# Kernel tuning notes

Hardware: AMD Instinct MI355X
Metric: run time of the kernel (lower is better)

Reference implementation:

```python
import jax, jax.numpy as jnp
import numpy as np

B, S, QD, KD = 8, 8192, 1024, 1024
AD = min(QD, KD)
EPS = 1e-5


def _ste(x, xq):
    # straight-through estimator: forward uses xq, gradient flows as identity
    return x + jax.lax.stop_gradient(xq - x)


def bitlinear(x, w, b):
    """BitNet b1.58-style BitLinear: ternary per-tensor weight quant,
    per-token int8 absmax activation quant, both with STE."""
    s = jnp.mean(jnp.abs(w)) + EPS                      # per-tensor weight scale
    wq = _ste(w, jnp.clip(jnp.round(w / s), -1.0, 1.0) * s)
    g = jnp.max(jnp.abs(x), axis=-1, keepdims=True) + EPS  # per-token act scale
    xq = _ste(x, jnp.clip(jnp.round(x * (127.0 / g)), -128.0, 127.0) * (g / 127.0))
    return jnp.matmul(xq, wq.T) + b


def setup_inputs() -> dict:
    key = jax.random.key(0)
    ks = jax.random.split(key, 6)
    sc = 0.02
    return {
        "query": jax.random.normal(ks[0], (B, QD), dtype=jnp.float32),
        "context_memory": jax.random.normal(ks[1], (B, S, KD), dtype=jnp.float32),
        "w_q": jax.random.normal(ks[2], (AD, QD), dtype=jnp.float32) * sc,
        "b_q": jnp.zeros((AD,), dtype=jnp.float32),
        "w_k": jax.random.normal(ks[3], (AD, KD), dtype=jnp.float32) * sc,
        "b_k": jnp.zeros((AD,), dtype=jnp.float32),
        "w_v": jax.random.normal(ks[4], (QD, KD), dtype=jnp.float32) * sc,
        "b_v": jnp.zeros((QD,), dtype=jnp.float32),
        "w_c": jax.random.normal(ks[5], (QD, 2 * QD), dtype=jnp.float32) * sc,
        "b_c": jnp.zeros((QD,), dtype=jnp.float32),
    }


def reference(query, context_memory, w_q, b_q, w_k, b_k, w_v, b_v, w_c, b_c):
    attention_dim = w_q.shape[0]
    q = bitlinear(query, w_q, b_q)                 # [B, A]
    k = bitlinear(context_memory, w_k, b_k)        # [B, S, A]
    v = bitlinear(context_memory, w_v, b_v)        # [B, S, QD]
    scores = jnp.einsum('ba,bsa->bs', q, k) / (attention_dim ** 0.5)
    attn = jax.nn.softmax(scores, axis=-1)         # [B, S]
    ctx = jnp.einsum('bs,bsq->bq', attn, v)        # [B, QD]
    combined = jnp.concatenate([query, ctx], axis=-1)  # [B, 2*QD]
    return bitlinear(combined, w_c, b_c)           # [B, QD]
```

## Files before the change

### kernel.cpp

```cpp
#include <hip/hip_runtime.h>
#include <hip/hip_bf16.h>
#include <math.h>

#define EPS 1e-5f

static constexpr int Bb = 8;
static constexpr int Ss = 8192;
static constexpr int Dd = 1024;
static constexpr int NW = 64;
static constexpr int NWv = NW * 4;
static constexpr int TOK = Ss / NWv;
static constexpr int NCH = 64;
static constexpr int RC = Dd / NCH;


__device__ __forceinline__ float blk_reduce(float v, bool ismax, volatile float* lds) {
#pragma unroll
  for (int msk = 32; msk; msk >>= 1) {
    float o = __shfl_xor(v, msk);
    v = ismax ? fmaxf(v, o) : (v + o);
  }
  int w = threadIdx.x >> 6;
  __syncthreads();
  if ((threadIdx.x & 63) == 0) lds[w] = v;
  __syncthreads();
  return ismax ? fmaxf(fmaxf(lds[0], lds[1]), fmaxf(lds[2], lds[3]))
               : (lds[0] + lds[1] + lds[2] + lds[3]);
}

__device__ __forceinline__ float wred_max(float v) {
#pragma unroll
  for (int msk = 32; msk; msk >>= 1) v = fmaxf(v, __shfl_xor(v, msk));
  return v;
}

__device__ __forceinline__ float wred_sum(float v) {
#pragma unroll
  for (int msk = 32; msk; msk >>= 1) v += __shfl_xor(v, msk);
  return v;
}

__device__ __forceinline__ float quantf(float x, float c) {
  return fminf(fmaxf(rintf(x * c), -128.f), 127.f);
}

__device__ __forceinline__ float ternf(float w, float s) {
  return fminf(fmaxf(rintf(w / s), -1.f), 1.f);
}


__global__ __launch_bounds__(256) void k_scales(
    const float* __restrict__ w0, const float* __restrict__ w1,
    const float* __restrict__ w2, const float* __restrict__ w3,
    double* __restrict__ part, float* __restrict__ scales, int* __restrict__ cnt)
{
  int seg = blockIdx.x >> 6;
  int blk = blockIdx.x & 63;
  const float* w = seg == 0 ? w0 : seg == 1 ? w1 : seg == 2 ? w2 : w3;
  int n4 = (seg == 3 ? (1024 * 2048) : (1024 * 1024)) >> 2;
  const float4* w4 = (const float4*)w;
  double acc = 0.0;
  for (int i = blk * 256 + threadIdx.x; i < n4; i += 64 * 256) {
    float4 v = w4[i];
    acc += (double)fabsf(v.x) + (double)fabsf(v.y)
         + (double)fabsf(v.z) + (double)fabsf(v.w);
  }
  __shared__ double sred[256];
  sred[threadIdx.x] = acc;
  __syncthreads();
  for (int s = 128; s > 0; s >>= 1) {
    if (threadIdx.x < s) sred[threadIdx.x] += sred[threadIdx.x + s];
    __syncthreads();
  }
  __shared__ int lastold;
  if (threadIdx.x == 0) {
    part[blockIdx.x] = sred[0];
    __threadfence();
    lastold = atomicAdd(cnt, 1);
  }
  __syncthreads();
  if (lastold == 255) {
    __threadfence();
    if (threadIdx.x < 4) {
      int sg = threadIdx.x;
      double s = 0.0;
      for (int i = 0; i < 64; i++) s += part[sg * 64 + i];
      double n = (sg == 3) ? 2097152.0 : 1048576.0;
      scales[sg] = (float)(s / n) + EPS;
    }
  }
}


__global__ __launch_bounds__(256) void k_qgemv(
    const float* __restrict__ query, const float* __restrict__ W,
    const float* __restrict__ bias, const float* __restrict__ scales,
    float* __restrict__ out)
{
  __shared__ float cs[Dd];
  __shared__ float red[4];
  int b = blockIdx.x >> 8, grp = blockIdx.x & 255;
  int tid = threadIdx.x, wv = tid >> 6, lane = tid & 63;
  float4 v = ((const float4*)(query + (size_t)b * Dd))[tid];
  float am = fmaxf(fmaxf(fabsf(v.x), fabsf(v.y)), fmaxf(fabsf(v.z), fabsf(v.w)));
  am = blk_reduce(am, true, red);
  float g = am + EPS;
  float c = 127.0f / g;
  float4 qv = make_float4(quantf(v.x, c), quantf(v.y, c), quantf(v.z, c), quantf(v.w, c));
  ((float4*)cs)[tid] = qv;
  __syncthreads();
  float s = scales[0];
  int o = grp * 4 + wv;
  const float4* wr = (const float4*)(W + (size_t)o * Dd);
  float acc = 0.f;
#pragma unroll
  for (int i = 0; i < 4; i++) {
    int idx = i * 64 + lane;
    float4 w4 = wr[idx];
    float4 a4 = ((const float4*)cs)[idx];
    acc += a4.x * ternf(w4.x, s) + a4.y * ternf(w4.y, s)
         + a4.z * ternf(w4.z, s) + a4.w * ternf(w4.w, s);
  }
  acc = wred_sum(acc);
  if (lane == 0) out[(size_t)b * Dd + o] = s * (g / 127.0f) * acc + bias[o];
}


__global__ __launch_bounds__(256) void k_qk(
    const float* __restrict__ q, const float* __restrict__ Wk,
    const float* __restrict__ bk, const float* __restrict__ scales,
    float* __restrict__ part, float* __restrict__ qk, float* __restrict__ qdotbk,
    int* __restrict__ cnt)
{
  __shared__ float qs[Bb * RC];
  int ch = blockIdx.x;
  int a0 = ch * RC;
  int tid = threadIdx.x;
  if (tid < Bb * RC) {
    int b = tid / RC, a = tid - b * RC;
    qs[tid] = q[(size_t)b * Dd + a0 + a];
  }
  __syncthreads();
  float s = scales[1];
  float4 acc[Bb];
#pragma unroll
  for (int b = 0; b < Bb; b++) acc[b] = make_float4(0.f, 0.f, 0.f, 0.f);
  const float4* Wr = (const float4*)(Wk + (size_t)a0 * Dd);
  for (int i = 0; i < RC; i++) {
    float4 w = Wr[(size_t)i * 256 + tid];
    float4 t;
    t.x = ternf(w.x, s); t.y = ternf(w.y, s);
    t.z = ternf(w.z, s); t.w = ternf(w.w, s);
#pragma unroll
    for (int b = 0; b < Bb; b++) {
      float qb = qs[b * RC + i];
      acc[b].x += qb * t.x; acc[b].y += qb * t.y;
      acc[b].z += qb * t.z; acc[b].w += qb * t.w;
    }
  }
#pragma unroll
  for (int b = 0; b < Bb; b++)
    ((float4*)part)[((size_t)ch * Bb + b) * 256 + tid] = acc[b];

  __threadfence();
  if (tid == 0) {
    atomicAdd(cnt, 1);
    while (__hip_atomic_load(cnt, __ATOMIC_ACQUIRE, __HIP_MEMORY_SCOPE_AGENT) < NCH) {
      __builtin_amdgcn_s_sleep(8);
    }
  }
  __syncthreads();
  __threadfence();

  int b = blockIdx.x >> 3, dc = blockIdx.x & 7;
  if (tid < 32) {
    int d4 = dc * 32 + tid;
    float4 a = make_float4(0.f, 0.f, 0.f, 0.f);
    for (int k = 0; k < NCH; k++) {
      float4 p = ((const float4*)part)[((size_t)k * Bb + b) * 256 + d4];
      a.x += p.x; a.y += p.y; a.z += p.z; a.w += p.w;
    }
    ((float4*)qk)[(size_t)b * 256 + d4] = make_float4(s * a.x, s * a.y, s * a.z, s * a.w);
  } else if (dc == 0 && tid >= 64 && tid < 128) {
    int lane = tid - 64;
    float p = 0.f;
    for (int a = lane; a < Dd; a += 64) p += q[(size_t)b * Dd + a] * bk[a];
    p = wred_sum(p);
    if (lane == 0) qdotbk[b] = p;
  }
}


__global__ __launch_bounds__(256) void k_pass(
    const float* __restrict__ X, const float* __restrict__ qk,
    const float* __restrict__ qdotbk,
    float* __restrict__ m_part, float* __restrict__ l_part,
    float* __restrict__ t_part)
{
  int b    = blockIdx.x >> 6;
  int wg   = blockIdx.x & 63;
  int wv   = threadIdx.x >> 6;
  int lane = threadIdx.x & 63;
  int widx = wg * 4 + wv;
  int s0   = widx * TOK;

  const float4* qkb = (const float4*)(qk + (size_t)b * Dd);
  float4 qv0 = qkb[lane], qv1 = qkb[64 + lane], qv2 = qkb[128 + lane], qv3 = qkb[192 + lane];
  float qb = qdotbk[b];
  const float4* Xw = (const float4*)(X + ((size_t)b * Ss + s0) * Dd);

  float m = -INFINITY, l = 0.f;
  float4 a0 = make_float4(0,0,0,0), a1 = a0, a2 = a0, a3 = a0;

  float4 x0 = Xw[lane], x1 = Xw[64 + lane], x2 = Xw[128 + lane], x3 = Xw[192 + lane];
  for (int i = 0; i < TOK; i++) {
    size_t nb = (size_t)((i + 1 < TOK) ? i + 1 : i) * 256;
    float4 n0 = Xw[nb + lane], n1 = Xw[nb + 64 + lane],
           n2 = Xw[nb + 128 + lane], n3 = Xw[nb + 192 + lane];

    float am = fmaxf(
      fmaxf(fmaxf(fmaxf(fabsf(x0.x), fabsf(x0.y)), fmaxf(fabsf(x0.z), fabsf(x0.w))),
            fmaxf(fmaxf(fabsf(x1.x), fabsf(x1.y)), fmaxf(fabsf(x1.z), fabsf(x1.w)))),
      fmaxf(fmaxf(fmaxf(fabsf(x2.x), fabsf(x2.y)), fmaxf(fabsf(x2.z), fabsf(x2.w))),
            fmaxf(fmaxf(fabsf(x3.x), fabsf(x3.y)), fmaxf(fabsf(x3.z), fabsf(x3.w)))));
    am = wred_max(am);
    float g = am + EPS;
    float c = 127.0f / g;
    float gi = g / 127.0f;

    float q00 = quantf(x0.x, c), q01 = quantf(x0.y, c), q02 = quantf(x0.z, c), q03 = quantf(x0.w, c);
    float q10 = quantf(x1.x, c), q11 = quantf(x1.y, c), q12 = quantf(x1.z, c), q13 = quantf(x1.w, c);
    float q20 = quantf(x2.x, c), q21 = quantf(x2.y, c), q22 = quantf(x2.z, c), q23 = quantf(x2.w, c);
    float q30 = quantf(x3.x, c), q31 = quantf(x3.y, c), q32 = quantf(x3.z, c), q33 = quantf(x3.w, c);

    float dt = q00 * qv0.x + q01 * qv0.y + q02 * qv0.z + q03 * qv0.w
             + q10 * qv1.x + q11 * qv1.y + q12 * qv1.z + q13 * qv1.w
             + q20 * qv2.x + q21 * qv2.y + q22 * qv2.z + q23 * qv2.w
             + q30 * qv3.x + q31 * qv3.y + q32 * qv3.z + q33 * qv3.w;
    dt = wred_sum(dt);

    float score = (dt * gi + qb) * 0.03125f;
    if (score <= m) {
      float p  = expf(score - m);
      l += p;
      float cf = p * gi;
      a0.x += cf * q00; a0.y += cf * q01; a0.z += cf * q02; a0.w += cf * q03;
      a1.x += cf * q10; a1.y += cf * q11; a1.z += cf * q12; a1.w += cf * q13;
      a2.x += cf * q20; a2.y += cf * q21; a2.z += cf * q22; a2.w += cf * q23;
      a3.x += cf * q30; a3.y += cf * q31; a3.z += cf * q32; a3.w += cf * q33;
    } else {
      float scl = expf(m - score);
      l = l * scl + 1.0f;
      float cf = gi;
      a0.x = a0.x * scl + cf * q00; a0.y = a0.y * scl + cf * q01;
      a0.z = a0.z * scl + cf * q02; a0.w = a0.w * scl + cf * q03;
      a1.x = a1.x * scl + cf * q10; a1.y = a1.y * scl + cf * q11;
      a1.z = a1.z * scl + cf * q12; a1.w = a1.w * scl + cf * q13;
      a2.x = a2.x * scl + cf * q20; a2.y = a2.y * scl + cf * q21;
      a2.z = a2.z * scl + cf * q22; a2.w = a2.w * scl + cf * q23;
      a3.x = a3.x * scl + cf * q30; a3.y = a3.y * scl + cf * q31;
      a3.z = a3.z * scl + cf * q32; a3.w = a3.w * scl + cf * q33;
      m = score;
    }
    x0 = n0; x1 = n1; x2 = n2; x3 = n3;
  }

  size_t pidx = (size_t)b * NWv + widx;
  float4* tpw = (float4*)t_part + (size_t)pidx * 256;
  tpw[lane] = a0; tpw[64 + lane] = a1; tpw[128 + lane] = a2; tpw[192 + lane] = a3;
  if (threadIdx.x == (unsigned)(wv << 6)) { m_part[pidx] = m; l_part[pidx] = l; }
}


__global__ __launch_bounds__(256) void k_comb(
    const float* __restrict__ m_part, const float* __restrict__ l_part,
    const float* __restrict__ t_part, float* __restrict__ t16,
    float* __restrict__ t, int* __restrict__ cnt)
{
  __shared__ float red[4];
  int b = blockIdx.x >> 4, k = blockIdx.x & 15;
  int tid = threadIdx.x;
  float mi = m_part[(size_t)b * NWv + tid];
  float M = blk_reduce(mi, true, red);
  float li = l_part[(size_t)b * NWv + tid] * expf(mi - M);
  float L = blk_reduce(li, false, red);

  float4 acc = make_float4(0,0,0,0);
  for (int i = 0; i < 16; i++) {
    size_t pi = (size_t)b * NWv + k * 16 + i;
    float w = expf(m_part[pi] - M);
    float4 tp = ((const float4*)t_part)[pi * 256 + tid];
    acc.x += w * tp.x; acc.y += w * tp.y; acc.z += w * tp.z; acc.w += w * tp.w;
  }
  ((float4*)t16)[((size_t)(b * 16 + k)) * 256 + tid] = acc;

  __shared__ int lastold;
  if (tid == 0) {
    __threadfence();
    lastold = atomicAdd(&cnt[b], 1);
  }
  __syncthreads();
  if (lastold == 15) {
    __threadfence();
    float invL = 1.0f / L;
    float4 a = make_float4(0,0,0,0);
    for (int kk = 0; kk < 16; kk++) {
      float4 v = ((const float4*)t16)[((size_t)(b * 16 + kk)) * 256 + tid];
      a.x += v.x; a.y += v.y; a.z += v.z; a.w += v.w;
    }
    ((float4*)t)[(size_t)b * 256 + tid] =
        make_float4(a.x * invL, a.y * invL, a.z * invL, a.w * invL);
  }
}


__global__ __launch_bounds__(256) void k_tern_gemv_f32(
    const float* __restrict__ act, const float* __restrict__ W,
    const float* __restrict__ bias, const float* __restrict__ scales, int sidx,
    float* __restrict__ out, int K, int N)
{
  int wave = blockIdx.x * 4 + (threadIdx.x >> 6);
  int lane = threadIdx.x & 63;
  int b = wave / N, o = wave - b * N;
  float s = scales[sidx];
  const float4* wr = (const float4*)(W + (size_t)o * K);
  const float4* ar = (const float4*)(act + (size_t)b * K);
  int n4 = K >> 2;
  float acc = 0.f;
  for (int i = lane; i < n4; i += 64) {
    float4 w4 = wr[i];
    float4 a4 = ar[i];
    acc += a4.x * ternf(w4.x, s) + a4.y * ternf(w4.y, s)
         + a4.z * ternf(w4.z, s) + a4.w * ternf(w4.w, s);
  }
  acc = wred_sum(acc);
  if (lane == 0) out[(size_t)b * N + o] = s * acc + bias[o];
}


__global__ __launch_bounds__(256) void k_final(
    const float* __restrict__ query, const float* __restrict__ ctx,
    const float* __restrict__ W, const float* __restrict__ bias,
    const float* __restrict__ scales, float* __restrict__ out)
{
  __shared__ float cs[2 * Dd];
  __shared__ float red[4];
  int b = blockIdx.x >> 8, grp = blockIdx.x & 255;
  int tid = threadIdx.x, wv = tid >> 6, lane = tid & 63;
  float4 vq = ((const float4*)(query + (size_t)b * Dd))[tid];
  float4 vc = ((const float4*)(ctx   + (size_t)b * Dd))[tid];
  float am = fmaxf(
      fmaxf(fmaxf(fabsf(vq.x), fabsf(vq.y)), fmaxf(fabsf(vq.z), fabsf(vq.w))),
      fmaxf(fmaxf(fabsf(vc.x), fabsf(vc.y)), fmaxf(fabsf(vc.z), fabsf(vc.w))));
  am = blk_reduce(am, true, red);
  float g = am + EPS;
  float c = 127.0f / g;
  ((float4*)cs)[tid] = make_float4(quantf(vq.x, c), quantf(vq.y, c), quantf(vq.z, c), quantf(vq.w, c));
  ((float4*)cs)[256 + tid] = make_float4(quantf(vc.x, c), quantf(vc.y, c), quantf(vc.z, c), quantf(vc.w, c));
  __syncthreads();
  float s = scales[3];
  int o = grp * 4 + wv;
  const float4* wr = (const float4*)(W + (size_t)o * 2 * Dd);
  float acc = 0.f;
#pragma unroll
  for (int i = 0; i < 8; i++) {
    int idx = i * 64 + lane;
    float4 w4 = wr[idx];
    float4 a4 = ((const float4*)cs)[idx];
    acc += a4.x * ternf(w4.x, s) + a4.y * ternf(w4.y, s)
         + a4.z * ternf(w4.z, s) + a4.w * ternf(w4.w, s);
  }
  acc = wred_sum(acc);
  if (lane == 0) out[(size_t)b * Dd + o] = s * (g / 127.0f) * acc + bias[o];
}


extern "C" void kernel_launch(void* const* d_in, const int* in_sizes, int n_in,
                              void* d_out, int out_size, void* d_ws, size_t ws_size,
                              hipStream_t stream)
{
  const float* query = (const float*)d_in[0];
  const float* X     = (const float*)d_in[1];
  const float* w_q   = (const float*)d_in[2];
  const float* b_q   = (const float*)d_in[3];
  const float* w_k   = (const float*)d_in[4];
  const float* b_k   = (const float*)d_in[5];
  const float* w_v   = (const float*)d_in[6];
  const float* b_v   = (const float*)d_in[7];
  const float* w_c   = (const float*)d_in[8];
  const float* b_c   = (const float*)d_in[9];
  float* out = (float*)d_out;
  char* ws = (char*)d_ws;

  size_t off = 0;
  auto alloc = [&](size_t bytes) -> size_t {
    size_t o = off;
    off += (bytes + 255) & ~(size_t)255;
    return o;
  };
  size_t o_cnt    = alloc(256);
  size_t o_part   = alloc(256 * sizeof(double));
  size_t o_scales = alloc(4 * sizeof(float));
  size_t o_q      = alloc((size_t)Bb * Dd * 4);
  size_t o_qk     = alloc((size_t)Bb * Dd * 4);
  size_t o_qbk    = alloc(Bb * sizeof(float));
  size_t o_t      = alloc((size_t)Bb * Dd * 4);
  size_t o_ctx    = alloc((size_t)Bb * Dd * 4);
  size_t o_t16    = alloc((size_t)Bb * 16 * Dd * 4);
  size_t o_qkp    = alloc((size_t)NCH * Bb * Dd * 4);
  size_t o_mp     = alloc((size_t)Bb * NWv * 4);
  size_t o_lp     = alloc((size_t)Bb * NWv * 4);
  size_t o_tp     = alloc((size_t)Bb * NWv * Dd * 4);
  (void)ws_size;

  int*    cnt    = (int*)(ws + o_cnt);
  double* part   = (double*)(ws + o_part);
  float*  scales = (float*)(ws + o_scales);
  float*  qv     = (float*)(ws + o_q);
  float*  qk     = (float*)(ws + o_qk);
  float*  qbk    = (float*)(ws + o_qbk);
  float*  tvec   = (float*)(ws + o_t);
  float*  ctx    = (float*)(ws + o_ctx);
  float*  t16    = (float*)(ws + o_t16);
  float*  qkp    = (float*)(ws + o_qkp);
  float*  mp     = (float*)(ws + o_mp);
  float*  lp     = (float*)(ws + o_lp);
  float*  tp     = (float*)(ws + o_tp);

  hipMemsetAsync(ws + o_cnt, 0, 256, stream);
  k_scales<<<256, 256, 0, stream>>>(w_q, w_k, w_v, w_c, part, scales, &cnt[0]);
  k_qgemv<<<Bb * 256, 256, 0, stream>>>(query, w_q, b_q, scales, qv);
  k_qk<<<NCH, 256, 0, stream>>>(qv, w_k, b_k, scales, qkp, qk, qbk, &cnt[1]);
  k_pass<<<Bb * NW, 256, 0, stream>>>(X, qk, qbk, mp, lp, tp);
  k_comb<<<Bb * 16, 256, 0, stream>>>(mp, lp, tp, t16, tvec, &cnt[2]);
  k_tern_gemv_f32<<<(Bb * Dd) / 4, 256, 0, stream>>>(tvec, w_v, b_v, scales, 2, ctx, Dd, Dd);
  k_final<<<Bb * 256, 256, 0, stream>>>(query, ctx, w_c, b_c, scales, out);
}
```

Baseline: 135.7 us.

## Fuse pre- and post-attention kernels into persistent kernels with grid spin barriers

Merges the scale reduction, q GEMV and q·Wk projection into one persistent 256-block kernel, and merges the softmax combine, Wv GEMV and final BitLinear into another, using atomic spin barriers between phases. The GEMVs now process all 8 batches per weight row so each ternarised weight is loaded once instead of eight times. The qk split grows to 128 chunks with a parallel reduction. This cuts launch count and weight traffic, but relies on all 256 blocks being co-resident and uses large LDS per block.

```diff
diff --git a/kernel.cpp b/kernel.cpp
--- a/kernel.cpp
+++ b/kernel.cpp
@@ -10,7 +10,7 @@
 static constexpr int NW = 64;
 static constexpr int NWv = NW * 4;
 static constexpr int TOK = Ss / NWv;
-static constexpr int NCH = 64;
+static constexpr int NCH = 128;
 static constexpr int RC = Dd / NCH;
 
 
@@ -48,145 +48,166 @@
   return fminf(fmaxf(rintf(w / s), -1.f), 1.f);
 }
 
-
-__global__ __launch_bounds__(256) void k_scales(
-    const float* __restrict__ w0, const float* __restrict__ w1,
-    const float* __restrict__ w2, const float* __restrict__ w3,
-    double* __restrict__ part, float* __restrict__ scales, int* __restrict__ cnt)
+__device__ __forceinline__ float4 tern4(float4 w, float s) {
+  return make_float4(ternf(w.x, s), ternf(w.y, s), ternf(w.z, s), ternf(w.w, s));
+}
+
+__device__ __forceinline__ float4 quant4(float4 v, float c) {
+  return make_float4(quantf(v.x, c), quantf(v.y, c), quantf(v.z, c), quantf(v.w, c));
+}
+
+__device__ __forceinline__ float dot4(float4 a, float4 b) {
+  return a.x * b.x + a.y * b.y + a.z * b.z + a.w * b.w;
+}
+
+__device__ __forceinline__ void gridspin(int* c, int target) {
+  __syncthreads();
+  if (threadIdx.x == 0) {
+    __threadfence();
+    atomicAdd(c, 1);
+    while (__hip_atomic_load(c, __ATOMIC_ACQUIRE, __HIP_MEMORY_SCOPE_AGENT) < target)
+      __builtin_amdgcn_s_sleep(8);
+  }
+  __syncthreads();
+  __threadfence();
+}
+
+
+__global__ __launch_bounds__(256) void k_pre(
+    const float* __restrict__ query,
+    const float* __restrict__ w_q, const float* __restrict__ b_q,
+    const float* __restrict__ w_k, const float* __restrict__ b_k,
+    const float* __restrict__ w_v, const float* __restrict__ w_c,
+    double* __restrict__ part, float* __restrict__ scales,
+    float* __restrict__ q, float* __restrict__ qkp,
+    float* __restrict__ qk, float* __restrict__ qdotbk, int* __restrict__ cnt)
 {
-  int seg = blockIdx.x >> 6;
-  int blk = blockIdx.x & 63;
-  const float* w = seg == 0 ? w0 : seg == 1 ? w1 : seg == 2 ? w2 : w3;
-  int n4 = (seg == 3 ? (1024 * 2048) : (1024 * 1024)) >> 2;
-  const float4* w4 = (const float4*)w;
-  double acc = 0.0;
-  for (int i = blk * 256 + threadIdx.x; i < n4; i += 64 * 256) {
-    float4 v = w4[i];
-    acc += (double)fabsf(v.x) + (double)fabsf(v.y)
-         + (double)fabsf(v.z) + (double)fabsf(v.w);
-  }
+  __shared__ float red[4];
   __shared__ double sred[256];
-  sred[threadIdx.x] = acc;
-  __syncthreads();
-  for (int s = 128; s > 0; s >>= 1) {
-    if (threadIdx.x < s) sred[threadIdx.x] += sred[threadIdx.x + s];
+  __shared__ float qs[Bb * Dd];
+  __shared__ float gsh[8];
+  __shared__ float ssh[4];
+  int tid = threadIdx.x;
+
+  {
+    int seg = blockIdx.x >> 6, blk = blockIdx.x & 63;
+    const float* w = seg == 0 ? w_q : seg == 1 ? w_k : seg == 2 ? w_v : w_c;
+    int n4 = (seg == 3 ? (1024 * 2048) : (1024 * 1024)) >> 2;
+    const float4* w4 = (const float4*)w;
+    double acc = 0.0;
+    for (int i = blk * 256 + tid; i < n4; i += 64 * 256) {
+      float4 v = w4[i];
+      acc += (double)fabsf(v.x) + (double)fabsf(v.y)
+           + (double)fabsf(v.z) + (double)fabsf(v.w);
+    }
+    sred[tid] = acc;
     __syncthreads();
-  }
-  __shared__ int lastold;
-  if (threadIdx.x == 0) {
-    part[blockIdx.x] = sred[0];
-    __threadfence();
-    lastold = atomicAdd(cnt, 1);
-  }
-  __syncthreads();
-  if (lastold == 255) {
-    __threadfence();
-    if (threadIdx.x < 4) {
-      int sg = threadIdx.x;
-      double s = 0.0;
-      for (int i = 0; i < 64; i++) s += part[sg * 64 + i];
-      double n = (sg == 3) ? 2097152.0 : 1048576.0;
-      scales[sg] = (float)(s / n) + EPS;
-    }
-  }
-}
-
-
-__global__ __launch_bounds__(256) void k_qgemv(
-    const float* __restrict__ query, const float* __restrict__ W,
-    const float* __restrict__ bias, const float* __restrict__ scales,
-    float* __restrict__ out)
-{
-  __shared__ float cs[Dd];
-  __shared__ float red[4];
-  int b = blockIdx.x >> 8, grp = blockIdx.x & 255;
-  int tid = threadIdx.x, wv = tid >> 6, lane = tid & 63;
-  float4 v = ((const float4*)(query + (size_t)b * Dd))[tid];
-  float am = fmaxf(fmaxf(fabsf(v.x), fabsf(v.y)), fmaxf(fabsf(v.z), fabsf(v.w)));
-  am = blk_reduce(am, true, red);
-  float g = am + EPS;
-  float c = 127.0f / g;
-  float4 qv = make_float4(quantf(v.x, c), quantf(v.y, c), quantf(v.z, c), quantf(v.w, c));
-  ((float4*)cs)[tid] = qv;
-  __syncthreads();
-  float s = scales[0];
-  int o = grp * 4 + wv;
-  const float4* wr = (const float4*)(W + (size_t)o * Dd);
-  float acc = 0.f;
-#pragma unroll
-  for (int i = 0; i < 4; i++) {
-    int idx = i * 64 + lane;
-    float4 w4 = wr[idx];
-    float4 a4 = ((const float4*)cs)[idx];
-    acc += a4.x * ternf(w4.x, s) + a4.y * ternf(w4.y, s)
-         + a4.z * ternf(w4.z, s) + a4.w * ternf(w4.w, s);
-  }
-  acc = wred_sum(acc);
-  if (lane == 0) out[(size_t)b * Dd + o] = s * (g / 127.0f) * acc + bias[o];
-}
-
-
-__global__ __launch_bounds__(256) void k_qk(
-    const float* __restrict__ q, const float* __restrict__ Wk,
-    const float* __restrict__ bk, const float* __restrict__ scales,
-    float* __restrict__ part, float* __restrict__ qk, float* __restrict__ qdotbk,
-    int* __restrict__ cnt)
-{
-  __shared__ float qs[Bb * RC];
-  int ch = blockIdx.x;
-  int a0 = ch * RC;
-  int tid = threadIdx.x;
-  if (tid < Bb * RC) {
-    int b = tid / RC, a = tid - b * RC;
-    qs[tid] = q[(size_t)b * Dd + a0 + a];
-  }
-  __syncthreads();
-  float s = scales[1];
-  float4 acc[Bb];
-#pragma unroll
-  for (int b = 0; b < Bb; b++) acc[b] = make_float4(0.f, 0.f, 0.f, 0.f);
-  const float4* Wr = (const float4*)(Wk + (size_t)a0 * Dd);
-  for (int i = 0; i < RC; i++) {
-    float4 w = Wr[(size_t)i * 256 + tid];
-    float4 t;
-    t.x = ternf(w.x, s); t.y = ternf(w.y, s);
-    t.z = ternf(w.z, s); t.w = ternf(w.w, s);
-#pragma unroll
-    for (int b = 0; b < Bb; b++) {
-      float qb = qs[b * RC + i];
-      acc[b].x += qb * t.x; acc[b].y += qb * t.y;
-      acc[b].z += qb * t.z; acc[b].w += qb * t.w;
-    }
-  }
-#pragma unroll
-  for (int b = 0; b < Bb; b++)
-    ((float4*)part)[((size_t)ch * Bb + b) * 256 + tid] = acc[b];
-
-  __threadfence();
-  if (tid == 0) {
-    atomicAdd(cnt, 1);
-    while (__hip_atomic_load(cnt, __ATOMIC_ACQUIRE, __HIP_MEMORY_SCOPE_AGENT) < NCH) {
-      __builtin_amdgcn_s_sleep(8);
-    }
-  }
-  __syncthreads();
-  __threadfence();
-
-  int b = blockIdx.x >> 3, dc = blockIdx.x & 7;
-  if (tid < 32) {
-    int d4 = dc * 32 + tid;
-    float4 a = make_float4(0.f, 0.f, 0.f, 0.f);
-    for (int k = 0; k < NCH; k++) {
-      float4 p = ((const float4*)part)[((size_t)k * Bb + b) * 256 + d4];
+    for (int s = 128; s > 0; s >>= 1) {
+      if (tid < s) sred[tid] += sred[tid + s];
+      __syncthreads();
+    }
+    if (tid == 0) part[blockIdx.x] = sred[0];
+  }
+  gridspin(&cnt[0], 256);
+
+  if (tid < 4) {
+    double s = 0.0;
+    for (int i = 0; i < 64; i++) s += part[tid * 64 + i];
+    double n = (tid == 3) ? 2097152.0 : 1048576.0;
+    ssh[tid] = (float)(s / n) + EPS;
+    if (blockIdx.x == 0) scales[tid] = ssh[tid];
+  }
+  __syncthreads();
+
+  for (int b = 0; b < 8; b++) {
+    float4 v = ((const float4*)(query + (size_t)b * Dd))[tid];
+    float am = fmaxf(fmaxf(fabsf(v.x), fabsf(v.y)), fmaxf(fabsf(v.z), fabsf(v.w)));
+    am = blk_reduce(am, true, red);
+    float g = am + EPS;
+    ((float4*)qs)[b * 256 + tid] = quant4(v, 127.0f / g);
+    if (tid == 0) gsh[b] = g;
+  }
+  __syncthreads();
+  {
+    float s0 = ssh[0];
+    int wv = tid >> 6, lane = tid & 63;
+    int o = blockIdx.x * 4 + wv;
+    const float4* wr = (const float4*)(w_q + (size_t)o * Dd);
+    float acc[8] = {0, 0, 0, 0, 0, 0, 0, 0};
+#pragma unroll
+    for (int i = 0; i < 4; i++) {
+      float4 t4 = tern4(wr[i * 64 + lane], s0);
+#pragma unroll
+      for (int b = 0; b < 8; b++)
+        acc[b] += dot4(((float4*)qs)[b * 256 + i * 64 + lane], t4);
+    }
+#pragma unroll
+    for (int b = 0; b < 8; b++) acc[b] = wred_sum(acc[b]);
+    if (lane == 0) {
+      float bq = b_q[o];
+#pragma unroll
+      for (int b = 0; b < 8; b++)
+        q[(size_t)b * Dd + o] = s0 * (gsh[b] / 127.0f) * acc[b] + bq;
+    }
+  }
+  gridspin(&cnt[1], 256);
+
+  float s1 = ssh[1];
+  if (blockIdx.x < NCH) {
+    __shared__ float qs2[Bb * RC];
+    int ch = blockIdx.x, a0 = ch * RC;
+    if (tid < Bb * RC) {
+      int b = tid / RC, a = tid - b * RC;
+      qs2[tid] = q[(size_t)b * Dd + a0 + a];
+    }
+    __syncthreads();
+    float4 acc4[8];
+#pragma unroll
+    for (int b = 0; b < 8; b++) acc4[b] = make_float4(0, 0, 0, 0);
+    const float4* Wr = (const float4*)(w_k + (size_t)a0 * Dd);
+    for (int i = 0; i < RC; i++) {
+      float4 t4 = tern4(Wr[(size_t)i * 256 + tid], s1);
+#pragma unroll
+      for (int b = 0; b < 8; b++) {
+        float qb = qs2[b * RC + i];
+        acc4[b].x += qb * t4.x; acc4[b].y += qb * t4.y;
+        acc4[b].z += qb * t4.z; acc4[b].w += qb * t4.w;
+      }
+    }
+#pragma unroll
+    for (int b = 0; b < 8; b++)
+      ((float4*)qkp)[((size_t)ch * Bb + b) * 256 + tid] = acc4[b];
+  }
+  gridspin(&cnt[2], 256);
+
+  if (blockIdx.x < 64) {
+    __shared__ float4 lred[8][32];
+    int b = blockIdx.x >> 3, dc = blockIdx.x & 7;
+    int col = tid & 31, kg = tid >> 5;
+    int d4 = dc * 32 + col;
+    float4 a = make_float4(0, 0, 0, 0);
+    for (int k = kg * 16; k < kg * 16 + 16; k++) {
+      float4 p = ((const float4*)qkp)[((size_t)k * Bb + b) * 256 + d4];
       a.x += p.x; a.y += p.y; a.z += p.z; a.w += p.w;
     }
-    ((float4*)qk)[(size_t)b * 256 + d4] = make_float4(s * a.x, s * a.y, s * a.z, s * a.w);
-  } else if (dc == 0 && tid >= 64 && tid < 128) {
-    int lane = tid - 64;
-    float p = 0.f;
-    for (int a = lane; a < Dd; a += 64) p += q[(size_t)b * Dd + a] * bk[a];
-    p = wred_sum(p);
-    if (lane == 0) qdotbk[b] = p;
+    lred[kg][col] = a;
+    __syncthreads();
+    if (kg == 0) {
+      float4 t = lred[0][col];
+#pragma unroll
+      for (int g = 1; g < 8; g++) {
+        float4 v = lred[g][col];
+        t.x += v.x; t.y += v.y; t.z += v.z; t.w += v.w;
+      }
+      ((float4*)qk)[(size_t)b * 256 + d4] =
+          make_float4(s1 * t.x, s1 * t.y, s1 * t.z, s1 * t.w);
+    } else if (dc == 0 && tid >= 192) {
+      int lane = tid - 192;
+      float p = 0.f;
+      for (int a2 = lane; a2 < Dd; a2 += 64) p += q[(size_t)b * Dd + a2] * b_k[a2];
+      p = wred_sum(p);
+      if (lane == 0) qdotbk[b] = p;
+    }
   }
 }
 
@@ -268,110 +289,134 @@
   size_t pidx = (size_t)b * NWv + widx;
   float4* tpw = (float4*)t_part + (size_t)pidx * 256;
   tpw[lane] = a0; tpw[64 + lane] = a1; tpw[128 + lane] = a2; tpw[192 + lane] = a3;
-  if (threadIdx.x == (unsigned)(wv << 6)) { m_part[pidx] = m; l_part[pidx] = l; }
-}
-
-
-__global__ __launch_bounds__(256) void k_comb(
+  if (lane == 0) { m_part[pidx] = m; l_part[pidx] = l; }
+}
+
+
+__global__ __launch_bounds__(256) void k_post(
+    const float* __restrict__ query,
     const float* __restrict__ m_part, const float* __restrict__ l_part,
-    const float* __restrict__ t_part, float* __restrict__ t16,
-    float* __restrict__ t, int* __restrict__ cnt)
+    const float* __restrict__ t_part,
+    const float* __restrict__ w_v, const float* __restrict__ b_v,
+    const float* __restrict__ w_c, const float* __restrict__ b_c,
+    const float* __restrict__ scales,
+    float* __restrict__ t32, float* __restrict__ ML,
+    float* __restrict__ tvec, float* __restrict__ ctx,
+    float* __restrict__ out, int* __restrict__ cnt)
 {
   __shared__ float red[4];
-  int b = blockIdx.x >> 4, k = blockIdx.x & 15;
+  __shared__ float cs[16384];
+  __shared__ float gsh[8];
   int tid = threadIdx.x;
-  float mi = m_part[(size_t)b * NWv + tid];
-  float M = blk_reduce(mi, true, red);
-  float li = l_part[(size_t)b * NWv + tid] * expf(mi - M);
-  float L = blk_reduce(li, false, red);
-
-  float4 acc = make_float4(0,0,0,0);
-  for (int i = 0; i < 16; i++) {
-    size_t pi = (size_t)b * NWv + k * 16 + i;
-    float w = expf(m_part[pi] - M);
-    float4 tp = ((const float4*)t_part)[pi * 256 + tid];
-    acc.x += w * tp.x; acc.y += w * tp.y; acc.z += w * tp.z; acc.w += w * tp.w;
-  }
-  ((float4*)t16)[((size_t)(b * 16 + k)) * 256 + tid] = acc;
-
-  __shared__ int lastold;
-  if (tid == 0) {
-    __threadfence();
-    lastold = atomicAdd(&cnt[b], 1);
-  }
-  __syncthreads();
-  if (lastold == 15) {
-    __threadfence();
-    float invL = 1.0f / L;
-    float4 a = make_float4(0,0,0,0);
-    for (int kk = 0; kk < 16; kk++) {
-      float4 v = ((const float4*)t16)[((size_t)(b * 16 + kk)) * 256 + tid];
+
+  {
+    int b = blockIdx.x >> 5, k = blockIdx.x & 31;
+    float mi = m_part[(size_t)b * NWv + tid];
+    float M = blk_reduce(mi, true, red);
+    float li = l_part[(size_t)b * NWv + tid] * expf(mi - M);
+    float L = blk_reduce(li, false, red);
+    float4 acc = make_float4(0, 0, 0, 0);
+    for (int i = 0; i < 8; i++) {
+      size_t pi = (size_t)b * NWv + k * 8 + i;
+      float w = expf(m_part[pi] - M);
+      float4 tp = ((const float4*)t_part)[pi * 256 + tid];
+      acc.x += w * tp.x; acc.y += w * tp.y; acc.z += w * tp.z; acc.w += w * tp.w;
+    }
+    ((float4*)t32)[((size_t)(b * 32 + k)) * 256 + tid] = acc;
+    if (k == 0 && tid == 0) { ML[b * 2] = M; ML[b * 2 + 1] = L; }
+  }
+  gridspin(&cnt[3], 256);
+
+  if (blockIdx.x < 64) {
+    __shared__ float4 lred[8][32];
+    int b = blockIdx.x >> 3, dc = blockIdx.x & 7;
+    int col = tid & 31, kg = tid >> 5;
+    int d4 = dc * 32 + col;
+    float4 a = make_float4(0, 0, 0, 0);
+    for (int kk = kg * 4; kk < kg * 4 + 4; kk++) {
+      float4 v = ((const float4*)t32)[((size_t)(b * 32 + kk)) * 256 + d4];
       a.x += v.x; a.y += v.y; a.z += v.z; a.w += v.w;
     }
-    ((float4*)t)[(size_t)b * 256 + tid] =
-        make_float4(a.x * invL, a.y * invL, a.z * invL, a.w * invL);
-  }
-}
-
-
-__global__ __launch_bounds__(256) void k_tern_gemv_f32(
-    const float* __restrict__ act, const float* __restrict__ W,
-    const float* __restrict__ bias, const float* __restrict__ scales, int sidx,
-    float* __restrict__ out, int K, int N)
-{
-  int wave = blockIdx.x * 4 + (threadIdx.x >> 6);
-  int lane = threadIdx.x & 63;
-  int b = wave / N, o = wave - b * N;
-  float s = scales[sidx];
-  const float4* wr = (const float4*)(W + (size_t)o * K);
-  const float4* ar = (const float4*)(act + (size_t)b * K);
-  int n4 = K >> 2;
-  float acc = 0.f;
-  for (int i = lane; i < n4; i += 64) {
-    float4 w4 = wr[i];
-    float4 a4 = ar[i];
-    acc += a4.x * ternf(w4.x, s) + a4.y * ternf(w4.y, s)
-         + a4.z * ternf(w4.z, s) + a4.w * ternf(w4.w, s);
-  }
-  acc = wred_sum(acc);
-  if (lane == 0) out[(size_t)b * N + o] = s * acc + bias[o];
-}
-
-
-__global__ __launch_bounds__(256) void k_final(
-    const float* __restrict__ query, const float* __restrict__ ctx,
-    const float* __restrict__ W, const float* __restrict__ bias,
-    const float* __restrict__ scales, float* __restrict__ out)
-{
-  __shared__ float cs[2 * Dd];
-  __shared__ float red[4];
-  int b = blockIdx.x >> 8, grp = blockIdx.x & 255;
-  int tid = threadIdx.x, wv = tid >> 6, lane = tid & 63;
-  float4 vq = ((const float4*)(query + (size_t)b * Dd))[tid];
-  float4 vc = ((const float4*)(ctx   + (size_t)b * Dd))[tid];
-  float am = fmaxf(
-      fmaxf(fmaxf(fabsf(vq.x), fabsf(vq.y)), fmaxf(fabsf(vq.z), fabsf(vq.w))),
-      fmaxf(fmaxf(fabsf(vc.x), fabsf(vc.y)), fmaxf(fabsf(vc.z), fabsf(vc.w))));
-  am = blk_reduce(am, true, red);
-  float g = am + EPS;
-  float c = 127.0f / g;
-  ((float4*)cs)[tid] = make_float4(quantf(vq.x, c), quantf(vq.y, c), quantf(vq.z, c), quantf(vq.w, c));
-  ((float4*)cs)[256 + tid] = make_float4(quantf(vc.x, c), quantf(vc.y, c), quantf(vc.z, c), quantf(vc.w, c));
-  __syncthreads();
-  float s = scales[3];
-  int o = grp * 4 + wv;
-  const float4* wr = (const float4*)(W + (size_t)o * 2 * Dd);
-  float acc = 0.f;
-#pragma unroll
-  for (int i = 0; i < 8; i++) {
-    int idx = i * 64 + lane;
-    float4 w4 = wr[idx];
-    float4 a4 = ((const float4*)cs)[idx];
-    acc += a4.x * ternf(w4.x, s) + a4.y * ternf(w4.y, s)
-         + a4.z * ternf(w4.z, s) + a4.w * ternf(w4.w, s);
-  }
-  acc = wred_sum(acc);
-  if (lane == 0) out[(size_t)b * Dd + o] = s * (g / 127.0f) * acc + bias[o];
+    lred[kg][col] = a;
+    __syncthreads();
+    if (kg == 0) {
+      float4 s = lred[0][col];
+#pragma unroll
+      for (int g = 1; g < 8; g++) {
+        float4 v = lred[g][col];
+        s.x += v.x; s.y += v.y; s.z += v.z; s.w += v.w;
+      }
+      float invL = 1.0f / ML[b * 2 + 1];
+      ((float4*)tvec)[(size_t)b * 256 + d4] =
+          make_float4(s.x * invL, s.y * invL, s.z * invL, s.w * invL);
+    }
+  }
+  gridspin(&cnt[4], 256);
+
+  for (int b = 0; b < 8; b++)
+    ((float4*)cs)[b * 256 + tid] = ((const float4*)tvec)[b * 256 + tid];
+  __syncthreads();
+  {
+    float s2 = scales[2];
+    int wv = tid >> 6, lane = tid & 63;
+    int o = blockIdx.x * 4 + wv;
+    const float4* wr = (const float4*)(w_v + (size_t)o * Dd);
+    float acc[8] = {0, 0, 0, 0, 0, 0, 0, 0};
+#pragma unroll
+    for (int i = 0; i < 4; i++) {
+      float4 t4 = tern4(wr[i * 64 + lane], s2);
+#pragma unroll
+      for (int b = 0; b < 8; b++)
+        acc[b] += dot4(((float4*)cs)[b * 256 + i * 64 + lane], t4);
+    }
+#pragma unroll
+    for (int b = 0; b < 8; b++) acc[b] = wred_sum(acc[b]);
+    if (lane == 0) {
+      float bv = b_v[o];
+#pragma unroll
+      for (int b = 0; b < 8; b++)
+        ctx[(size_t)b * Dd + o] = s2 * acc[b] + bv;
+    }
+  }
+  gridspin(&cnt[5], 256);
+
+  __syncthreads();
+  for (int b = 0; b < 8; b++) {
+    float4 vq = ((const float4*)(query + (size_t)b * Dd))[tid];
+    float4 vc = ((const float4*)(ctx   + (size_t)b * Dd))[tid];
+    float am = fmaxf(
+        fmaxf(fmaxf(fabsf(vq.x), fabsf(vq.y)), fmaxf(fabsf(vq.z), fabsf(vq.w))),
+        fmaxf(fmaxf(fabsf(vc.x), fabsf(vc.y)), fmaxf(fabsf(vc.z), fabsf(vc.w))));
+    am = blk_reduce(am, true, red);
+    float g = am + EPS;
+    float c = 127.0f / g;
+    ((float4*)cs)[b * 512 + tid]       = quant4(vq, c);
+    ((float4*)cs)[b * 512 + 256 + tid] = quant4(vc, c);
+    if (tid == 0) gsh[b] = g;
+  }
+  __syncthreads();
+  {
+    float s3 = scales[3];
+    int wv = tid >> 6, lane = tid & 63;
+    int o = blockIdx.x * 4 + wv;
+    const float4* wr = (const float4*)(w_c + (size_t)o * 2 * Dd);
+    float acc[8] = {0, 0, 0, 0, 0, 0, 0, 0};
+#pragma unroll
+    for (int i = 0; i < 8; i++) {
+      float4 t4 = tern4(wr[i * 64 + lane], s3);
+#pragma unroll
+      for (int b = 0; b < 8; b++)
+        acc[b] += dot4(((float4*)cs)[b * 512 + i * 64 + lane], t4);
+    }
+#pragma unroll
+    for (int b = 0; b < 8; b++) acc[b] = wred_sum(acc[b]);
+    if (lane == 0) {
+      float bc = b_c[o];
+#pragma unroll
+      for (int b = 0; b < 8; b++)
+        out[(size_t)b * Dd + o] = s3 * (gsh[b] / 127.0f) * acc[b] + bc;
+    }
+  }
 }
 
 
@@ -406,7 +451,8 @@
   size_t o_qbk    = alloc(Bb * sizeof(float));
   size_t o_t      = alloc((size_t)Bb * Dd * 4);
   size_t o_ctx    = alloc((size_t)Bb * Dd * 4);
-  size_t o_t16    = alloc((size_t)Bb * 16 * Dd * 4);
+  size_t o_ML     = alloc(Bb * 2 * sizeof(float));
+  size_t o_t32    = alloc((size_t)Bb * 32 * Dd * 4);
   size_t o_qkp    = alloc((size_t)NCH * Bb * Dd * 4);
   size_t o_mp     = alloc((size_t)Bb * NWv * 4);
   size_t o_lp     = alloc((size_t)Bb * NWv * 4);
@@ -421,18 +467,17 @@
   float*  qbk    = (float*)(ws + o_qbk);
   float*  tvec   = (float*)(ws + o_t);
   float*  ctx    = (float*)(ws + o_ctx);
-  float*  t16    = (float*)(ws + o_t16);
+  float*  ML     = (float*)(ws + o_ML);
+  float*  t32    = (float*)(ws + o_t32);
   float*  qkp    = (float*)(ws + o_qkp);
   float*  mp     = (float*)(ws + o_mp);
   float*  lp     = (float*)(ws + o_lp);
   float*  tp     = (float*)(ws + o_tp);
 
   hipMemsetAsync(ws + o_cnt, 0, 256, stream);
-  k_scales<<<256, 256, 0, stream>>>(w_q, w_k, w_v, w_c, part, scales, &cnt[0]);
-  k_qgemv<<<Bb * 256, 256, 0, stream>>>(query, w_q, b_q, scales, qv);
-  k_qk<<<NCH, 256, 0, stream>>>(qv, w_k, b_k, scales, qkp, qk, qbk, &cnt[1]);
+  k_pre<<<256, 256, 0, stream>>>(query, w_q, b_q, w_k, b_k, w_v, w_c,
+                                 part, scales, qv, qkp, qk, qbk, cnt);
   k_pass<<<Bb * NW, 256, 0, stream>>>(X, qk, qbk, mp, lp, tp);
-  k_comb<<<Bb * 16, 256, 0, stream>>>(mp, lp, tp, t16, tvec, &cnt[2]);
-  k_tern_gemv_f32<<<(Bb * Dd) / 4, 256, 0, stream>>>(tvec, w_v, b_v, scales, 2, ctx, Dd, Dd);
-  k_final<<<Bb * 256, 256, 0, stream>>>(query, ctx, w_c, b_c, scales, out);
-}
+  k_post<<<256, 256, 0, stream>>>(query, mp, lp, tp, w_v, b_v, w_c, b_c,
+                                  scales, t32, ML, tvec, ctx, out, cnt);
+}
```

After: 303.1 us. 2.23x slower.

## Batch all eight rows per block in ternary GEMVs to reuse weight loads

Applied to the files above, without the earlier changes.

The q, v and final ternary GEMV kernels now have each block handle all 8 batch rows for its 4 output columns. Quantized activations for every batch go into shared memory, and each weight row is read and ternarized once instead of once per batch. This cuts weight traffic and ternarize work by up to 8x, at the cost of fewer blocks (256), more shared memory (up to 64KB in k_final), and a serial per-batch absmax reduction loop in each block.

```diff
diff --git a/kernel.cpp b/kernel.cpp
--- a/kernel.cpp
+++ b/kernel.cpp
@@ -46,6 +46,18 @@
 
 __device__ __forceinline__ float ternf(float w, float s) {
   return fminf(fmaxf(rintf(w / s), -1.f), 1.f);
+}
+
+__device__ __forceinline__ float4 tern4(float4 w, float s) {
+  return make_float4(ternf(w.x, s), ternf(w.y, s), ternf(w.z, s), ternf(w.w, s));
+}
+
+__device__ __forceinline__ float4 quant4(float4 v, float c) {
+  return make_float4(quantf(v.x, c), quantf(v.y, c), quantf(v.z, c), quantf(v.w, c));
+}
+
+__device__ __forceinline__ float dot4(float4 a, float4 b) {
+  return a.x * b.x + a.y * b.y + a.z * b.z + a.w * b.w;
 }
 
 
@@ -97,32 +109,38 @@
     const float* __restrict__ bias, const float* __restrict__ scales,
     float* __restrict__ out)
 {
-  __shared__ float cs[Dd];
+  __shared__ float qs[Bb * Dd];
   __shared__ float red[4];
-  int b = blockIdx.x >> 8, grp = blockIdx.x & 255;
+  __shared__ float gsh[8];
   int tid = threadIdx.x, wv = tid >> 6, lane = tid & 63;
-  float4 v = ((const float4*)(query + (size_t)b * Dd))[tid];
-  float am = fmaxf(fmaxf(fabsf(v.x), fabsf(v.y)), fmaxf(fabsf(v.z), fabsf(v.w)));
-  am = blk_reduce(am, true, red);
-  float g = am + EPS;
-  float c = 127.0f / g;
-  float4 qv = make_float4(quantf(v.x, c), quantf(v.y, c), quantf(v.z, c), quantf(v.w, c));
-  ((float4*)cs)[tid] = qv;
-  __syncthreads();
-  float s = scales[0];
-  int o = grp * 4 + wv;
+  for (int b = 0; b < 8; b++) {
+    float4 v = ((const float4*)(query + (size_t)b * Dd))[tid];
+    float am = fmaxf(fmaxf(fabsf(v.x), fabsf(v.y)), fmaxf(fabsf(v.z), fabsf(v.w)));
+    am = blk_reduce(am, true, red);
+    float g = am + EPS;
+    ((float4*)qs)[b * 256 + tid] = quant4(v, 127.0f / g);
+    if (tid == 0) gsh[b] = g;
+  }
+  __syncthreads();
+  float s0 = scales[0];
+  int o = blockIdx.x * 4 + wv;
   const float4* wr = (const float4*)(W + (size_t)o * Dd);
-  float acc = 0.f;
+  float acc[8] = {0, 0, 0, 0, 0, 0, 0, 0};
 #pragma unroll
   for (int i = 0; i < 4; i++) {
-    int idx = i * 64 + lane;
-    float4 w4 = wr[idx];
-    float4 a4 = ((const float4*)cs)[idx];
-    acc += a4.x * ternf(w4.x, s) + a4.y * ternf(w4.y, s)
-         + a4.z * ternf(w4.z, s) + a4.w * ternf(w4.w, s);
-  }
-  acc = wred_sum(acc);
-  if (lane == 0) out[(size_t)b * Dd + o] = s * (g / 127.0f) * acc + bias[o];
+    float4 t4 = tern4(wr[i * 64 + lane], s0);
+#pragma unroll
+    for (int b = 0; b < 8; b++)
+      acc[b] += dot4(((float4*)qs)[b * 256 + i * 64 + lane], t4);
+  }
+#pragma unroll
+  for (int b = 0; b < 8; b++) acc[b] = wred_sum(acc[b]);
+  if (lane == 0) {
+    float bq = bias[o];
+#pragma unroll
+    for (int b = 0; b < 8; b++)
+      out[(size_t)b * Dd + o] = s0 * (gsh[b] / 127.0f) * acc[b] + bq;
+  }
 }
 
 
@@ -147,15 +165,12 @@
   for (int b = 0; b < Bb; b++) acc[b] = make_float4(0.f, 0.f, 0.f, 0.f);
   const float4* Wr = (const float4*)(Wk + (size_t)a0 * Dd);
   for (int i = 0; i < RC; i++) {
-    float4 w = Wr[(size_t)i * 256 + tid];
-    float4 t;
-    t.x = ternf(w.x, s); t.y = ternf(w.y, s);
-    t.z = ternf(w.z, s); t.w = ternf(w.w, s);
+    float4 t4 = tern4(Wr[(size_t)i * 256 + tid], s);
 #pragma unroll
     for (int b = 0; b < Bb; b++) {
       float qb = qs[b * RC + i];
-      acc[b].x += qb * t.x; acc[b].y += qb * t.y;
-      acc[b].z += qb * t.z; acc[b].w += qb * t.w;
+      acc[b].x += qb * t4.x; acc[b].y += qb * t4.y;
+      acc[b].z += qb * t4.z; acc[b].w += qb * t4.w;
     }
   }
 #pragma unroll
@@ -165,9 +180,8 @@
   __threadfence();
   if (tid == 0) {
     atomicAdd(cnt, 1);
-    while (__hip_atomic_load(cnt, __ATOMIC_ACQUIRE, __HIP_MEMORY_SCOPE_AGENT) < NCH) {
+    while (__hip_atomic_load(cnt, __ATOMIC_ACQUIRE, __HIP_MEMORY_SCOPE_AGENT) < NCH)
       __builtin_amdgcn_s_sleep(8);
-    }
   }
   __syncthreads();
   __threadfence();
@@ -184,7 +198,7 @@
   } else if (dc == 0 && tid >= 64 && tid < 128) {
     int lane = tid - 64;
     float p = 0.f;
-    for (int a = lane; a < Dd; a += 64) p += q[(size_t)b * Dd + a] * bk[a];
+    for (int a2 = lane; a2 < Dd; a2 += 64) p += q[(size_t)b * Dd + a2] * bk[a2];
     p = wred_sum(p);
     if (lane == 0) qdotbk[b] = p;
   }
@@ -268,7 +282,7 @@
   size_t pidx = (size_t)b * NWv + widx;
   float4* tpw = (float4*)t_part + (size_t)pidx * 256;
   tpw[lane] = a0; tpw[64 + lane] = a1; tpw[128 + lane] = a2; tpw[192 + lane] = a3;
-  if (threadIdx.x == (unsigned)(wv << 6)) { m_part[pidx] = m; l_part[pidx] = l; }
+  if (lane == 0) { m_part[pidx] = m; l_part[pidx] = l; }
 }
 
 
@@ -314,27 +328,35 @@
 }
 
 
-__global__ __launch_bounds__(256) void k_tern_gemv_f32(
+__global__ __launch_bounds__(256) void k_vgemv(
     const float* __restrict__ act, const float* __restrict__ W,
-    const float* __restrict__ bias, const float* __restrict__ scales, int sidx,
-    float* __restrict__ out, int K, int N)
-{
-  int wave = blockIdx.x * 4 + (threadIdx.x >> 6);
-  int lane = threadIdx.x & 63;
-  int b = wave / N, o = wave - b * N;
-  float s = scales[sidx];
-  const float4* wr = (const float4*)(W + (size_t)o * K);
-  const float4* ar = (const float4*)(act + (size_t)b * K);
-  int n4 = K >> 2;
-  float acc = 0.f;
-  for (int i = lane; i < n4; i += 64) {
-    float4 w4 = wr[i];
-    float4 a4 = ar[i];
-    acc += a4.x * ternf(w4.x, s) + a4.y * ternf(w4.y, s)
-         + a4.z * ternf(w4.z, s) + a4.w * ternf(w4.w, s);
-  }
-  acc = wred_sum(acc);
-  if (lane == 0) out[(size_t)b * N + o] = s * acc + bias[o];
+    const float* __restrict__ bias, const float* __restrict__ scales,
+    float* __restrict__ out)
+{
+  __shared__ float cs[Bb * Dd];
+  int tid = threadIdx.x, wv = tid >> 6, lane = tid & 63;
+  for (int b = 0; b < 8; b++)
+    ((float4*)cs)[b * 256 + tid] = ((const float4*)act)[b * 256 + tid];
+  __syncthreads();
+  float s2 = scales[2];
+  int o = blockIdx.x * 4 + wv;
+  const float4* wr = (const float4*)(W + (size_t)o * Dd);
+  float acc[8] = {0, 0, 0, 0, 0, 0, 0, 0};
+#pragma unroll
+  for (int i = 0; i < 4; i++) {
+    float4 t4 = tern4(wr[i * 64 + lane], s2);
+#pragma unroll
+    for (int b = 0; b < 8; b++)
+      acc[b] += dot4(((float4*)cs)[b * 256 + i * 64 + lane], t4);
+  }
+#pragma unroll
+  for (int b = 0; b < 8; b++) acc[b] = wred_sum(acc[b]);
+  if (lane == 0) {
+    float bv = bias[o];
+#pragma unroll
+    for (int b = 0; b < 8; b++)
+      out[(size_t)b * Dd + o] = s2 * acc[b] + bv;
+  }
 }
 
 
@@ -343,35 +365,43 @@
     const float* __restrict__ W, const float* __restrict__ bias,
     const float* __restrict__ scales, float* __restrict__ out)
 {
-  __shared__ float cs[2 * Dd];
+  __shared__ float cs[Bb * 2 * Dd];
   __shared__ float red[4];
-  int b = blockIdx.x >> 8, grp = blockIdx.x & 255;
+  __shared__ float gsh[8];
   int tid = threadIdx.x, wv = tid >> 6, lane = tid & 63;
-  float4 vq = ((const float4*)(query + (size_t)b * Dd))[tid];
-  float4 vc = ((const float4*)(ctx   + (size_t)b * Dd))[tid];
-  float am = fmaxf(
-      fmaxf(fmaxf(fabsf(vq.x), fabsf(vq.y)), fmaxf(fabsf(vq.z), fabsf(vq.w))),
-      fmaxf(fmaxf(fabsf(vc.x), fabsf(vc.y)), fmaxf(fabsf(vc.z), fabsf(vc.w))));
-  am = blk_reduce(am, true, red);
-  float g = am + EPS;
-  float c = 127.0f / g;
-  ((float4*)cs)[tid] = make_float4(quantf(vq.x, c), quantf(vq.y, c), quantf(vq.z, c), quantf(vq.w, c));
-  ((float4*)cs)[256 + tid] = make_float4(quantf(vc.x, c), quantf(vc.y, c), quantf(vc.z, c), quantf(vc.w, c));
-  __syncthreads();
-  float s = scales[3];
-  int o = grp * 4 + wv;
+  for (int b = 0; b < 8; b++) {
+    float4 vq = ((const float4*)(query + (size_t)b * Dd))[tid];
+    float4 vc = ((const float4*)(ctx   + (size_t)b * Dd))[tid];
+    float am = fmaxf(
+        fmaxf(fmaxf(fabsf(vq.x), fabsf(vq.y)), fmaxf(fabsf(vq.z), fabsf(vq.w))),
+        fmaxf(fmaxf(fabsf(vc.x), fabsf(vc.y)), fmaxf(fabsf(vc.z), fabsf(vc.w))));
+    am = blk_reduce(am, true, red);
+    float g = am + EPS;
+    float c = 127.0f / g;
+    ((float4*)cs)[b * 512 + tid]       = quant4(vq, c);
+    ((float4*)cs)[b * 512 + 256 + tid] = quant4(vc, c);
+    if (tid == 0) gsh[b] = g;
+  }
+  __syncthreads();
+  float s3 = scales[3];
+  int o = blockIdx.x * 4 + wv;
   const float4* wr = (const float4*)(W + (size_t)o * 2 * Dd);
-  float acc = 0.f;
+  float acc[8] = {0, 0, 0, 0, 0, 0, 0, 0};
 #pragma unroll
   for (int i = 0; i < 8; i++) {
-    int idx = i * 64 + lane;
-    float4 w4 = wr[idx];
-    float4 a4 = ((const float4*)cs)[idx];
-    acc += a4.x * ternf(w4.x, s) + a4.y * ternf(w4.y, s)
-         + a4.z * ternf(w4.z, s) + a4.w * ternf(w4.w, s);
-  }
-  acc = wred_sum(acc);
-  if (lane == 0) out[(size_t)b * Dd + o] = s * (g / 127.0f) * acc + bias[o];
+    float4 t4 = tern4(wr[i * 64 + lane], s3);
+#pragma unroll
+    for (int b = 0; b < 8; b++)
+      acc[b] += dot4(((float4*)cs)[b * 512 + i * 64 + lane], t4);
+  }
+#pragma unroll
+  for (int b = 0; b < 8; b++) acc[b] = wred_sum(acc[b]);
+  if (lane == 0) {
+    float bc = bias[o];
+#pragma unroll
+    for (int b = 0; b < 8; b++)
+      out[(size_t)b * Dd + o] = s3 * (gsh[b] / 127.0f) * acc[b] + bc;
+  }
 }
 
 
@@ -429,10 +459,10 @@
 
   hipMemsetAsync(ws + o_cnt, 0, 256, stream);
   k_scales<<<256, 256, 0, stream>>>(w_q, w_k, w_v, w_c, part, scales, &cnt[0]);
-  k_qgemv<<<Bb * 256, 256, 0, stream>>>(query, w_q, b_q, scales, qv);
+  k_qgemv<<<256, 256, 0, stream>>>(query, w_q, b_q, scales, qv);
   k_qk<<<NCH, 256, 0, stream>>>(qv, w_k, b_k, scales, qkp, qk, qbk, &cnt[1]);
   k_pass<<<Bb * NW, 256, 0, stream>>>(X, qk, qbk, mp, lp, tp);
   k_comb<<<Bb * 16, 256, 0, stream>>>(mp, lp, tp, t16, tvec, &cnt[2]);
-  k_tern_gemv_f32<<<(Bb * Dd) / 4, 256, 0, stream>>>(tvec, w_v, b_v, scales, 2, ctx, Dd, Dd);
-  k_final<<<Bb * 256, 256, 0, stream>>>(query, ctx, w_c, b_c, scales, out);
-}
+  k_vgemv<<<256, 256, 0, stream>>>(tvec, w_v, b_v, scales, ctx);
+  k_final<<<256, 256, 0, stream>>>(query, ctx, w_c, b_c, scales, out);
+}
```

New measurement: 140.5 us. 3.5% more time.
